# Performance work log

Measured on AMD Instinct MI355X. Metric: run time of the kernel, lower is better.

## Reference

```python
import jax, jax.numpy as jnp
import numpy as np

HID, H, D = 256, 8, 32
NU, NI, NT, NIM = 20000, 50000, 50000, 50000
EB, ETA, EIA = 400000, 200000, 200000
R_ALPHA = 0.5


def setup_inputs() -> dict:
    key = jax.random.key(0)
    ks = iter(jax.random.split(key, 64))
    def nrm(shape, s):
        return (jax.random.normal(next(ks), shape, jnp.float32) * s)
    inp = {}
    inp['x_user'] = nrm((NU, HID), 1.0)
    inp['x_item'] = nrm((NI, HID), 1.0)
    inp['x_taste'] = nrm((NT, HID), 1.0)
    inp['x_image'] = nrm((NIM, HID), 1.0)
    inp['eb_src'] = jax.random.randint(next(ks), (EB,), 0, NU)
    inp['eb_dst'] = jax.random.randint(next(ks), (EB,), 0, NI)
    inp['eta_src'] = jax.random.randint(next(ks), (ETA,), 0, NT)
    inp['eta_dst'] = jax.random.randint(next(ks), (ETA,), 0, NI)
    inp['eia_src'] = jax.random.randint(next(ks), (EIA,), 0, NIM)
    inp['eia_dst'] = jax.random.randint(next(ks), (EIA,), 0, NI)
    wscale = 1.0 / np.sqrt(HID)
    for t in ['user', 'taste', 'image']:
        inp[f'Wk_{t}'] = nrm((HID, HID), wscale)
        inp[f'bk_{t}'] = jnp.zeros((HID,), jnp.float32)
        inp[f'Wv_{t}'] = nrm((HID, HID), wscale)
        inp[f'bv_{t}'] = jnp.zeros((HID,), jnp.float32)
    inp['Wq_item'] = nrm((HID, HID), wscale)
    inp['bq_item'] = jnp.zeros((HID,), jnp.float32)
    rscale = 1.0 / np.sqrt(D)
    for r in ['buys', 'ta', 'ia']:
        inp[f'a_{r}'] = nrm((H, D, D), rscale)   # HGT a_rel (attention) per head
        inp[f'm_{r}'] = nrm((H, D, D), rscale)   # HGT m_rel (message) per head
        inp[f'p_{r}'] = jnp.ones((H,), jnp.float32)  # relation priority
    inp['Wo_item'] = nrm((HID, HID), wscale)
    inp['bo_item'] = jnp.zeros((HID,), jnp.float32)
    inp['skip_item'] = jnp.array(1.0, jnp.float32)  # PyG init: skip=1
    return inp


def _proj(x, W, b):
    return (x @ W + b).reshape(-1, H, D)


def _edge_attend(q, k, v, a_rel, m_rel, p_rel, src, dst):
    # per-source-node relation transforms (cheaper than per-edge when E > N)
    kr = jnp.einsum('nhd,hde->nhe', k, a_rel)
    vr = jnp.einsum('nhd,hde->nhe', v, m_rel)
    logits = jnp.einsum('ehd,ehd->eh', q[dst], kr[src]) * p_rel / np.sqrt(D)  # [E,H]
    mx = jax.ops.segment_max(logits, dst, num_segments=NI)
    ex = jnp.exp(logits - mx[dst])
    den = jax.ops.segment_sum(ex, dst, num_segments=NI)
    alpha = ex / (den[dst] + 1e-16)
    return jax.ops.segment_sum(vr[src] * alpha[:, :, None], dst, num_segments=NI)


def reference(x_user, x_item, x_taste, x_image,
              eb_src, eb_dst, eta_src, eta_dst, eia_src, eia_dst,
              Wk_user, bk_user, Wv_user, bv_user,
              Wk_taste, bk_taste, Wv_taste, bv_taste,
              Wk_image, bk_image, Wv_image, bv_image,
              Wq_item, bq_item,
              a_buys, m_buys, p_buys, a_ta, m_ta, p_ta, a_ia, m_ia, p_ia,
              Wo_item, bo_item, skip_item):
    q = _proj(x_item, Wq_item, bq_item)
    agg = _edge_attend(q, _proj(x_user, Wk_user, bk_user), _proj(x_user, Wv_user, bv_user),
                       a_buys, m_buys, p_buys, eb_src, eb_dst)
    agg = agg + _edge_attend(q, _proj(x_taste, Wk_taste, bk_taste), _proj(x_taste, Wv_taste, bv_taste),
                             a_ta, m_ta, p_ta, eta_src, eta_dst)
    agg = agg + _edge_attend(q, _proj(x_image, Wk_image, bk_image), _proj(x_image, Wv_image, bv_image),
                             a_ia, m_ia, p_ia, eia_src, eia_dst)
    out = jax.nn.gelu(agg).reshape(-1, HID) @ Wo_item + bo_item
    s = jax.nn.sigmoid(skip_item)
    out = s * out + (1.0 - s) * x_item          # HGTConv skip connection
    return out * (1.0 - R_ALPHA) + x_item * R_ALPHA  # MultiModalFusionGAT residual blend
```

## Files before the change

kernel.cpp:

```cpp
#include <hip/hip_runtime.h>
#include <stdint.h>

namespace {

constexpr int cNI  = 50000;
constexpr int cNU  = 20000;
constexpr int cNT  = 50000;
constexpr int cNIM = 50000;
constexpr int cEB  = 400000;
constexpr int cETA = 200000;
constexpr int cEIA = 200000;
constexpr int cTOT = 3 * cNI;

typedef __bf16 bf16x8 __attribute__((ext_vector_type(8)));
typedef float  floatx4 __attribute__((ext_vector_type(4)));

__device__ __forceinline__ float bf2f(unsigned short u) {
  union { unsigned int i; float f; } c;
  c.i = ((unsigned int)u) << 16;
  return c.f;
}
__device__ __forceinline__ unsigned short f2bf(float f) {
  union { float f; unsigned int i; } c;
  c.f = f;
  unsigned int u = c.i;
  u += 0x7fffu + ((u >> 16) & 1u);
  return (unsigned short)(u >> 16);
}
__device__ __forceinline__ float gelu_f(float x) {
  float u = 0.7978845608028654f * (x + 0.044715f * x * x * x);
  float e = __expf(2.f * u);
  float t = 1.f - 2.f / (e + 1.f);
  return 0.5f * x * (1.f + t);
}

__global__ __launch_bounds__(256) void combine_kernel(
    const float* __restrict__ Wk_u, const float* __restrict__ bk_u,
    const float* __restrict__ Wv_u, const float* __restrict__ bv_u,
    const float* __restrict__ Wk_t, const float* __restrict__ bk_t,
    const float* __restrict__ Wv_t, const float* __restrict__ bv_t,
    const float* __restrict__ Wk_i, const float* __restrict__ bk_i,
    const float* __restrict__ Wv_i, const float* __restrict__ bv_i,
    const float* __restrict__ a_b, const float* __restrict__ m_b, const float* __restrict__ p_b,
    const float* __restrict__ a_t, const float* __restrict__ m_t, const float* __restrict__ p_t,
    const float* __restrict__ a_i, const float* __restrict__ m_i, const float* __restrict__ p_i,
    const float* __restrict__ Wq, const float* __restrict__ bq,
    const float* __restrict__ Wo, const float* __restrict__ bo,
    unsigned short* __restrict__ WkvT_u, float* __restrict__ bkv_u,
    unsigned short* __restrict__ WkvT_t, float* __restrict__ bkv_t,
    unsigned short* __restrict__ WkvT_i, float* __restrict__ bkv_i,
    unsigned short* __restrict__ WqT, float* __restrict__ bqf,
    unsigned short* __restrict__ WoT, float* __restrict__ bof)
{
  int idx = blockIdx.x * 256 + threadIdx.x;
  if (idx < 3 * 512 * 256) {
    int rel  = idx >> 17;
    int rem  = idx & 131071;
    int jrow = rem >> 8;
    int k    = rem & 255;
    int isv  = jrow >> 8;
    int j = jrow & 255, h = j >> 5, e = j & 31;
    const float *W, *bin, *A, *pp;
    unsigned short* Wout; float* bout;
    if (rel == 0)      { W = isv ? Wv_u : Wk_u; bin = isv ? bv_u : bk_u; A = isv ? m_b : a_b; pp = p_b; Wout = WkvT_u; bout = bkv_u; }
    else if (rel == 1) { W = isv ? Wv_t : Wk_t; bin = isv ? bv_t : bk_t; A = isv ? m_t : a_t; pp = p_t; Wout = WkvT_t; bout = bkv_t; }
    else               { W = isv ? Wv_i : Wk_i; bin = isv ? bv_i : bk_i; A = isv ? m_i : a_i; pp = p_i; Wout = WkvT_i; bout = bkv_i; }
    float scale = isv ? 1.0f : pp[h] * 0.17677669529663687f;
    const float* wrow = W + k * 256 + h * 32;
    const float* acol = A + h * 1024 + e;
    float acc = 0.f;
    for (int d = 0; d < 32; ++d) acc += wrow[d] * acol[d * 32];
    Wout[jrow * 256 + k] = f2bf(acc * scale);
    if (k == 0) {
      const float* brow = bin + h * 32;
      float bacc = 0.f;
      for (int d = 0; d < 32; ++d) bacc += brow[d] * acol[d * 32];
      bout[jrow] = bacc * scale;
    }
  } else if (idx < 3 * 512 * 256 + 2 * 256 * 256) {
    int rem = idx - 3 * 512 * 256;
    int which = rem >> 16;
    int r2 = rem & 65535;
    int j = r2 >> 8, k = r2 & 255;
    if (which == 0) { WqT[j * 256 + k] = f2bf(Wq[k * 256 + j]); if (k == 0) bqf[j] = bq[j]; }
    else            { WoT[j * 256 + k] = f2bf(Wo[k * 256 + j]); if (k == 0) bof[j] = bo[j]; }
  }
}

template <int MODE>
__global__ __launch_bounds__(256) void gemm_bt_kernel(
    const void* __restrict__ Avp, const unsigned short* __restrict__ BT,
    const float* __restrict__ bias, void* __restrict__ Cvp,
    int M, int N,
    const float* __restrict__ xres, const float* __restrict__ skipp)
{
  __shared__ __align__(16) unsigned short As[64][40];
  __shared__ __align__(16) unsigned short Bs[64][40];
  const int tid = threadIdx.x;
  const int m0 = blockIdx.x * 64;
  const int n0 = blockIdx.y * 64;
  const int wave = tid >> 6, lane = tid & 63;
  const int wm = (wave >> 1) * 32, wn = (wave & 1) * 32;
  const int quad = lane >> 4, l16 = lane & 15;
  floatx4 acc00 = {0.f,0.f,0.f,0.f}, acc01 = {0.f,0.f,0.f,0.f};
  floatx4 acc10 = {0.f,0.f,0.f,0.f}, acc11 = {0.f,0.f,0.f,0.f};
  const int lrow = tid >> 2, lq = tid & 3;
  const int grow = m0 + lrow;
  for (int kt = 0; kt < 256; kt += 32) {
    uint4 av = make_uint4(0u, 0u, 0u, 0u);
    if (MODE == 0) {
      const float* Af = (const float*)Avp;
      if (grow < M) {
        const float4* ap = (const float4*)(Af + (size_t)grow * 256 + kt + lq * 8);
        float4 f0 = ap[0], f1 = ap[1];
        av.x = (unsigned int)f2bf(f0.x) | ((unsigned int)f2bf(f0.y) << 16);
        av.y = (unsigned int)f2bf(f0.z) | ((unsigned int)f2bf(f0.w) << 16);
        av.z = (unsigned int)f2bf(f1.x) | ((unsigned int)f2bf(f1.y) << 16);
        av.w = (unsigned int)f2bf(f1.z) | ((unsigned int)f2bf(f1.w) << 16);
      }
    } else {
      const unsigned short* Ab = (const unsigned short*)Avp;
      if (grow < M) av = *(const uint4*)(Ab + (size_t)grow * 256 + kt + lq * 8);
    }
    uint4 bv = *(const uint4*)(BT + (size_t)(n0 + lrow) * 256 + kt + lq * 8);
    *(uint4*)(&As[lrow][lq * 8]) = av;
    *(uint4*)(&Bs[lrow][lq * 8]) = bv;
    __syncthreads();
    bf16x8 a0 = *(const bf16x8*)(&As[wm + l16][quad * 8]);
    bf16x8 a1 = *(const bf16x8*)(&As[wm + 16 + l16][quad * 8]);
    bf16x8 b0 = *(const bf16x8*)(&Bs[wn + l16][quad * 8]);
    bf16x8 b1 = *(const bf16x8*)(&Bs[wn + 16 + l16][quad * 8]);
    acc00 = __builtin_amdgcn_mfma_f32_16x16x32_bf16(a0, b0, acc00, 0, 0, 0);
    acc01 = __builtin_amdgcn_mfma_f32_16x16x32_bf16(a0, b1, acc01, 0, 0, 0);
    acc10 = __builtin_amdgcn_mfma_f32_16x16x32_bf16(a1, b0, acc10, 0, 0, 0);
    acc11 = __builtin_amdgcn_mfma_f32_16x16x32_bf16(a1, b1, acc11, 0, 0, 0);
    __syncthreads();
  }
  float s = 0.f;
  if (MODE == 1) s = 1.f / (1.f + __expf(-skipp[0]));
  floatx4 accs[2][2] = {{acc00, acc01}, {acc10, acc11}};
  for (int mi = 0; mi < 2; ++mi) {
    for (int ni = 0; ni < 2; ++ni) {
      int col = n0 + wn + ni * 16 + l16;
      int rbase = m0 + wm + mi * 16 + quad * 4;
      float bcol = bias[col];
      for (int r = 0; r < 4; ++r) {
        int row = rbase + r;
        if (row < M) {
          float v = accs[mi][ni][r] + bcol;
          if (MODE == 0) {
            ((unsigned short*)Cvp)[(size_t)row * N + col] = f2bf(v);
          } else {
            float xi = xres[(size_t)row * 256 + col];
            float o = s * v + (1.f - s) * xi;
            ((float*)Cvp)[(size_t)row * 256 + col] = 0.5f * o + 0.5f * xi;
          }
        }
      }
    }
  }
}

__global__ __launch_bounds__(256) void hist_kernel(
    const int* __restrict__ ebd, const int* __restrict__ etd, const int* __restrict__ eid,
    int* __restrict__ cnt)
{
  int i = blockIdx.x * 256 + threadIdx.x;
  if (i < cEB)  atomicAdd(&cnt[ebd[i]], 1);
  if (i < cETA) atomicAdd(&cnt[cNI + etd[i]], 1);
  if (i < cEIA) atomicAdd(&cnt[2 * cNI + eid[i]], 1);
}

__global__ __launch_bounds__(256) void scan1_kernel(
    const int* __restrict__ cnt, int* __restrict__ tpre, int* __restrict__ bsum)
{
  __shared__ int wsum[4];
  const int tid = threadIdx.x, lane = tid & 63, wid = tid >> 6;
  const int base = blockIdx.x * 4096 + tid * 16;
  int s = 0;
  if (base + 16 <= cTOT) {
    const int4* p4 = (const int4*)(cnt + base);
    for (int j = 0; j < 4; ++j) { int4 v = p4[j]; s += v.x + v.y + v.z + v.w; }
  } else {
    for (int j = 0; j < 16; ++j) { int i = base + j; if (i < cTOT) s += cnt[i]; }
  }
  int x = s;
  for (int d = 1; d < 64; d <<= 1) { int t = __shfl_up(x, d, 64); if (lane >= d) x += t; }
  if (lane == 63) wsum[wid] = x;
  __syncthreads();
  int wb = 0;
  for (int w = 0; w < 4; ++w) { int v = wsum[w]; if (w < wid) wb += v; }
  tpre[blockIdx.x * 256 + tid] = wb + x - s;
  if (tid == 255) bsum[blockIdx.x] = wb + x;
}

__global__ __launch_bounds__(64) void scan2_kernel(
    const int* __restrict__ bsum, int* __restrict__ bbase, int* __restrict__ off,
    int nblocks)
{
  const int lane = threadIdx.x;
  int v = (lane < nblocks) ? bsum[lane] : 0;
  int x = v;
  for (int d = 1; d < 64; d <<= 1) { int t = __shfl_up(x, d, 64); if (lane >= d) x += t; }
  if (lane < nblocks) bbase[lane] = x - v;
  if (lane == 0) {
    off[cNI] = cEB;
    off[(cNI + 1) + cNI] = cETA;
    off[2 * (cNI + 1) + cNI] = cEIA;
  }
}

__global__ __launch_bounds__(256) void scan3_kernel(
    const int* __restrict__ cnt, const int* __restrict__ tpre,
    const int* __restrict__ bbase, int* __restrict__ off, int* __restrict__ cur)
{
  const int tid = threadIdx.x;
  const int b = blockIdx.x;
  const int base = b * 4096 + tid * 16;
  int run = bbase[b] + tpre[b * 256 + tid];
  for (int j = 0; j < 16; ++j) {
    int i = base + j;
    if (i >= cTOT) break;
    int rel = (i >= 2 * cNI) ? 2 : (i >= cNI ? 1 : 0);
    int pos = i - rel * cNI;
    int relbase = (rel == 0) ? 0 : (rel == 1) ? cEB : (cEB + cETA);
    int val = run - relbase;
    off[rel * (cNI + 1) + pos] = val;
    cur[rel * cNI + pos] = val;
    run += cnt[i];
  }
}

__global__ __launch_bounds__(256) void scatter_kernel(
    const int* __restrict__ ebs, const int* __restrict__ ebd,
    const int* __restrict__ ets, const int* __restrict__ etd,
    const int* __restrict__ eis, const int* __restrict__ eid,
    int* __restrict__ cur,
    int* __restrict__ ss_b, int* __restrict__ ss_t, int* __restrict__ ss_i)
{
  int i = blockIdx.x * 256 + threadIdx.x;
  if (i < cEB)  { int p = atomicAdd(&cur[ebd[i]], 1);           ss_b[p] = ebs[i]; }
  if (i < cETA) { int p = atomicAdd(&cur[cNI + etd[i]], 1);     ss_t[p] = ets[i]; }
  if (i < cEIA) { int p = atomicAdd(&cur[2 * cNI + eid[i]], 1); ss_i[p] = eis[i]; }
}

__global__ __launch_bounds__(256) void attend_kernel(
    const unsigned short* __restrict__ q,
    const unsigned short* __restrict__ kv_u,
    const unsigned short* __restrict__ kv_t,
    const unsigned short* __restrict__ kv_i,
    const int* __restrict__ off,
    const int* __restrict__ ss_b, const int* __restrict__ ss_t, const int* __restrict__ ss_i,
    unsigned short* __restrict__ gout)
{
  const int wave = threadIdx.x >> 6;
  const int lane = threadIdx.x & 63;
  const int item = blockIdx.x * 4 + wave;
  if (item >= cNI) return;
  ushort4 qu = ((const ushort4*)(q + (size_t)item * 256))[lane];
  const float q0 = bf2f(qu.x), q1 = bf2f(qu.y), q2 = bf2f(qu.z), q3 = bf2f(qu.w);
  float t0 = 0.f, t1 = 0.f, t2 = 0.f, t3 = 0.f;

#define EDGE_DOT(ku, vu, den, a0, a1, a2, a3)                                \
  {                                                                          \
    float p = bf2f(ku.x) * q0 + bf2f(ku.y) * q1 +                            \
              bf2f(ku.z) * q2 + bf2f(ku.w) * q3;                             \
    p += __shfl_xor(p, 1, 8);                                                \
    p += __shfl_xor(p, 2, 8);                                                \
    p += __shfl_xor(p, 4, 8);                                                \
    p = fminf(fmaxf(p, -30.f), 30.f);                                        \
    float ex = __expf(p);                                                    \
    den += ex;                                                               \
    a0 += ex * bf2f(vu.x); a1 += ex * bf2f(vu.y);                            \
    a2 += ex * bf2f(vu.z); a3 += ex * bf2f(vu.w);                            \
  }

#define DO_REL(KV, OFFBASE, SS, NSRC)                                        \
  {                                                                          \
    int e0 = off[(OFFBASE) + item];                                          \
    int e1 = off[(OFFBASE) + item + 1];                                      \
    float den = 0.f, a0 = 0.f, a1 = 0.f, a2 = 0.f, a3 = 0.f;                 \
    int e = e0;                                                              \
    for (; e + 2 <= e1; e += 2) {                                            \
      int s0 = SS[e], s1 = SS[e + 1];                                        \
      if ((unsigned)s0 >= (unsigned)(NSRC)) s0 = 0;                          \
      if ((unsigned)s1 >= (unsigned)(NSRC)) s1 = 0;                          \
      const ushort4* b0p = (const ushort4*)((KV) + (size_t)s0 * 512);        \
      const ushort4* b1p = (const ushort4*)((KV) + (size_t)s1 * 512);        \
      ushort4 k0 = b0p[lane];                                                \
      ushort4 v0 = b0p[64 + lane];                                           \
      ushort4 k1 = b1p[lane];                                                \
      ushort4 v1 = b1p[64 + lane];                                           \
      EDGE_DOT(k0, v0, den, a0, a1, a2, a3)                                  \
      EDGE_DOT(k1, v1, den, a0, a1, a2, a3)                                  \
    }                                                                        \
    if (e < e1) {                                                            \
      int s0 = SS[e];                                                        \
      if ((unsigned)s0 >= (unsigned)(NSRC)) s0 = 0;                          \
      const ushort4* b0p = (const ushort4*)((KV) + (size_t)s0 * 512);        \
      ushort4 k0 = b0p[lane];                                                \
      ushort4 v0 = b0p[64 + lane];                                           \
      EDGE_DOT(k0, v0, den, a0, a1, a2, a3)                                  \
    }                                                                        \
    float inv = 1.f / (den + 1e-16f);                                        \
    t0 += a0 * inv; t1 += a1 * inv; t2 += a2 * inv; t3 += a3 * inv;          \
  }

  DO_REL(kv_u, 0, ss_b, cNU)
  DO_REL(kv_t, (cNI + 1), ss_t, cNT)
  DO_REL(kv_i, 2 * (cNI + 1), ss_i, cNIM)
#undef DO_REL
#undef EDGE_DOT

  ushort4 o;
  o.x = f2bf(gelu_f(t0));
  o.y = f2bf(gelu_f(t1));
  o.z = f2bf(gelu_f(t2));
  o.w = f2bf(gelu_f(t3));
  ((ushort4*)(gout + (size_t)item * 256))[lane] = o;
}

}

extern "C" void kernel_launch(void* const* d_in, const int* in_sizes, int n_in,
                              void* d_out, int out_size, void* d_ws, size_t ws_size,
                              hipStream_t stream) {
  (void)in_sizes; (void)n_in; (void)out_size; (void)ws_size;
  const float* x_user  = (const float*)d_in[0];
  const float* x_item  = (const float*)d_in[1];
  const float* x_taste = (const float*)d_in[2];
  const float* x_image = (const float*)d_in[3];
  const int* eb_src  = (const int*)d_in[4];
  const int* eb_dst  = (const int*)d_in[5];
  const int* eta_src = (const int*)d_in[6];
  const int* eta_dst = (const int*)d_in[7];
  const int* eia_src = (const int*)d_in[8];
  const int* eia_dst = (const int*)d_in[9];
  const float* Wk_u = (const float*)d_in[10];
  const float* bk_u = (const float*)d_in[11];
  const float* Wv_u = (const float*)d_in[12];
  const float* bv_u = (const float*)d_in[13];
  const float* Wk_t = (const float*)d_in[14];
  const float* bk_t = (const float*)d_in[15];
  const float* Wv_t = (const float*)d_in[16];
  const float* bv_t = (const float*)d_in[17];
  const float* Wk_i = (const float*)d_in[18];
  const float* bk_i = (const float*)d_in[19];
  const float* Wv_i = (const float*)d_in[20];
  const float* bv_i = (const float*)d_in[21];
  const float* Wq   = (const float*)d_in[22];
  const float* bq   = (const float*)d_in[23];
  const float* a_b  = (const float*)d_in[24];
  const float* m_b  = (const float*)d_in[25];
  const float* p_b  = (const float*)d_in[26];
  const float* a_t  = (const float*)d_in[27];
  const float* m_t  = (const float*)d_in[28];
  const float* p_t  = (const float*)d_in[29];
  const float* a_i  = (const float*)d_in[30];
  const float* m_i  = (const float*)d_in[31];
  const float* p_i  = (const float*)d_in[32];
  const float* Wo   = (const float*)d_in[33];
  const float* bo   = (const float*)d_in[34];
  const float* skip = (const float*)d_in[35];

  char* p = (char*)d_ws;
  auto alloc = [&](size_t n) -> char* {
    char* r = p;
    p += (n + 255) & ~(size_t)255;
    return r;
  };
  unsigned short* q      = (unsigned short*)alloc((size_t)cNI * 256 * 2);
  unsigned short* kv_u   = (unsigned short*)alloc((size_t)cNU * 512 * 2);
  unsigned short* kv_t   = (unsigned short*)alloc((size_t)cNT * 512 * 2);
  unsigned short* kv_i   = (unsigned short*)alloc((size_t)cNIM * 512 * 2);
  unsigned short* gagg   = (unsigned short*)alloc((size_t)cNI * 256 * 2);
  unsigned short* WkvT_u = (unsigned short*)alloc(512 * 256 * 2);
  unsigned short* WkvT_t = (unsigned short*)alloc(512 * 256 * 2);
  unsigned short* WkvT_i = (unsigned short*)alloc(512 * 256 * 2);
  unsigned short* WqT    = (unsigned short*)alloc(256 * 256 * 2);
  unsigned short* WoT    = (unsigned short*)alloc(256 * 256 * 2);
  float* bkv_u = (float*)alloc(512 * 4);
  float* bkv_t = (float*)alloc(512 * 4);
  float* bkv_i = (float*)alloc(512 * 4);
  float* bqf   = (float*)alloc(256 * 4);
  float* bof   = (float*)alloc(256 * 4);
  int* cnt   = (int*)alloc((size_t)cTOT * 4);
  int* off   = (int*)alloc((size_t)3 * (cNI + 1) * 4);
  int* cur   = (int*)alloc((size_t)cTOT * 4);
  int* tpre  = (int*)alloc((size_t)37 * 256 * 4);
  int* bsum  = (int*)alloc(64 * 4);
  int* bbase = (int*)alloc(64 * 4);
  int* ss_b = (int*)alloc((size_t)cEB * 4);
  int* ss_t = (int*)alloc((size_t)cETA * 4);
  int* ss_i = (int*)alloc((size_t)cEIA * 4);

  hipMemsetAsync(cnt, 0, (size_t)cTOT * 4, stream);

  combine_kernel<<<2048, 256, 0, stream>>>(
      Wk_u, bk_u, Wv_u, bv_u, Wk_t, bk_t, Wv_t, bv_t, Wk_i, bk_i, Wv_i, bv_i,
      a_b, m_b, p_b, a_t, m_t, p_t, a_i, m_i, p_i,
      Wq, bq, Wo, bo,
      WkvT_u, bkv_u, WkvT_t, bkv_t, WkvT_i, bkv_i, WqT, bqf, WoT, bof);

  gemm_bt_kernel<0><<<dim3(782, 4), 256, 0, stream>>>(x_item, WqT, bqf, q, cNI, 256, nullptr, nullptr);
  gemm_bt_kernel<0><<<dim3(313, 8), 256, 0, stream>>>(x_user, WkvT_u, bkv_u, kv_u, cNU, 512, nullptr, nullptr);
  gemm_bt_kernel<0><<<dim3(782, 8), 256, 0, stream>>>(x_taste, WkvT_t, bkv_t, kv_t, cNT, 512, nullptr, nullptr);
  gemm_bt_kernel<0><<<dim3(782, 8), 256, 0, stream>>>(x_image, WkvT_i, bkv_i, kv_i, cNIM, 512, nullptr, nullptr);

  hist_kernel<<<1563, 256, 0, stream>>>(eb_dst, eta_dst, eia_dst, cnt);
  scan1_kernel<<<37, 256, 0, stream>>>(cnt, tpre, bsum);
  scan2_kernel<<<1, 64, 0, stream>>>(bsum, bbase, off, 37);
  scan3_kernel<<<37, 256, 0, stream>>>(cnt, tpre, bbase, off, cur);
  scatter_kernel<<<1563, 256, 0, stream>>>(eb_src, eb_dst, eta_src, eta_dst, eia_src, eia_dst,
                                           cur, ss_b, ss_t, ss_i);

  attend_kernel<<<12500, 256, 0, stream>>>(q, kv_u, kv_t, kv_i, off, ss_b, ss_t, ss_i, gagg);

  gemm_bt_kernel<1><<<dim3(782, 4), 256, 0, stream>>>(gagg, WoT, bof, d_out,
                                                      cNI, 256, x_item, skip);
}
```

Before: 699.6 us.

## Batch projection GEMMs into one strip kernel, merge scan passes, unroll attend loop

The four projection GEMMs now run as a single grouped launch. Each block loads a full 64x256 A strip once into shared memory, keeps it in registers, and loops over all N tiles. This stops the fp32 input from being re-read and re-converted once per N tile, and it cuts launch count. The scan2 kernel is removed: each scan3 block sums the preceding block totals itself. The attend loop now processes four edges at a time to keep more gathers in flight. In exchange, the change uses more shared memory and registers per block and launches fewer blocks, which may lower occupancy.

```diff
diff --git a/kernel.cpp b/kernel.cpp
--- a/kernel.cpp
+++ b/kernel.cpp
@@ -11,6 +11,12 @@
 constexpr int cETA = 200000;
 constexpr int cEIA = 200000;
 constexpr int cTOT = 3 * cNI;
+constexpr int cSCANB = 37;
+
+constexpr int cSQ  = (cNI  + 63) / 64;
+constexpr int cSU  = (cNU  + 63) / 64;
+constexpr int cST  = (cNT  + 63) / 64;
+constexpr int cSIM = (cNIM + 63) / 64;
 
 typedef __bf16 bf16x8 __attribute__((ext_vector_type(8)));
 typedef float  floatx4 __attribute__((ext_vector_type(4)));
@@ -88,30 +94,42 @@
 }
 
 template <int MODE>
-__global__ __launch_bounds__(256) void gemm_bt_kernel(
-    const void* __restrict__ Avp, const unsigned short* __restrict__ BT,
-    const float* __restrict__ bias, void* __restrict__ Cvp,
-    int M, int N,
+__global__ __launch_bounds__(256) void gemm_strip_kernel(
+    const void* __restrict__ A0, const unsigned short* __restrict__ B0,
+    const float* __restrict__ bias0, void* __restrict__ C0, int M0, int N0,
+    const void* __restrict__ A1, const unsigned short* __restrict__ B1,
+    const float* __restrict__ bias1, void* __restrict__ C1, int M1, int N1,
+    const void* __restrict__ A2, const unsigned short* __restrict__ B2,
+    const float* __restrict__ bias2, void* __restrict__ C2, int M2, int N2,
+    const void* __restrict__ A3, const unsigned short* __restrict__ B3,
+    const float* __restrict__ bias3, void* __restrict__ C3, int M3, int N3,
     const float* __restrict__ xres, const float* __restrict__ skipp)
 {
-  __shared__ __align__(16) unsigned short As[64][40];
-  __shared__ __align__(16) unsigned short Bs[64][40];
+  __shared__ __align__(16) unsigned short As[8][64][40];
+  __shared__ __align__(16) unsigned short Bs[8][64][40];
+
+  const void* Avp; const unsigned short* BT; const float* bias; void* Cvp;
+  int M, N, strip;
+  int b = blockIdx.x;
+  if (MODE == 1 || b < cSQ)            { Avp = A0; BT = B0; bias = bias0; Cvp = C0; M = M0; N = N0; strip = b; }
+  else if (b < cSQ + cSU)              { Avp = A1; BT = B1; bias = bias1; Cvp = C1; M = M1; N = N1; strip = b - cSQ; }
+  else if (b < cSQ + cSU + cST)        { Avp = A2; BT = B2; bias = bias2; Cvp = C2; M = M2; N = N2; strip = b - cSQ - cSU; }
+  else                                 { Avp = A3; BT = B3; bias = bias3; Cvp = C3; M = M3; N = N3; strip = b - cSQ - cSU - cST; }
+
   const int tid = threadIdx.x;
-  const int m0 = blockIdx.x * 64;
-  const int n0 = blockIdx.y * 64;
+  const int m0 = strip * 64;
   const int wave = tid >> 6, lane = tid & 63;
   const int wm = (wave >> 1) * 32, wn = (wave & 1) * 32;
   const int quad = lane >> 4, l16 = lane & 15;
-  floatx4 acc00 = {0.f,0.f,0.f,0.f}, acc01 = {0.f,0.f,0.f,0.f};
-  floatx4 acc10 = {0.f,0.f,0.f,0.f}, acc11 = {0.f,0.f,0.f,0.f};
   const int lrow = tid >> 2, lq = tid & 3;
   const int grow = m0 + lrow;
-  for (int kt = 0; kt < 256; kt += 32) {
+
+#pragma unroll
+  for (int kt = 0; kt < 8; ++kt) {
     uint4 av = make_uint4(0u, 0u, 0u, 0u);
     if (MODE == 0) {
-      const float* Af = (const float*)Avp;
       if (grow < M) {
-        const float4* ap = (const float4*)(Af + (size_t)grow * 256 + kt + lq * 8);
+        const float4* ap = (const float4*)((const float*)Avp + (size_t)grow * 256 + kt * 32 + lq * 8);
         float4 f0 = ap[0], f1 = ap[1];
         av.x = (unsigned int)f2bf(f0.x) | ((unsigned int)f2bf(f0.y) << 16);
         av.y = (unsigned int)f2bf(f0.z) | ((unsigned int)f2bf(f0.w) << 16);
@@ -119,45 +137,69 @@
         av.w = (unsigned int)f2bf(f1.z) | ((unsigned int)f2bf(f1.w) << 16);
       }
     } else {
-      const unsigned short* Ab = (const unsigned short*)Avp;
-      if (grow < M) av = *(const uint4*)(Ab + (size_t)grow * 256 + kt + lq * 8);
+      if (grow < M) av = *(const uint4*)((const unsigned short*)Avp + (size_t)grow * 256 + kt * 32 + lq * 8);
     }
-    uint4 bv = *(const uint4*)(BT + (size_t)(n0 + lrow) * 256 + kt + lq * 8);
-    *(uint4*)(&As[lrow][lq * 8]) = av;
-    *(uint4*)(&Bs[lrow][lq * 8]) = bv;
-    __syncthreads();
-    bf16x8 a0 = *(const bf16x8*)(&As[wm + l16][quad * 8]);
-    bf16x8 a1 = *(const bf16x8*)(&As[wm + 16 + l16][quad * 8]);
-    bf16x8 b0 = *(const bf16x8*)(&Bs[wn + l16][quad * 8]);
-    bf16x8 b1 = *(const bf16x8*)(&Bs[wn + 16 + l16][quad * 8]);
-    acc00 = __builtin_amdgcn_mfma_f32_16x16x32_bf16(a0, b0, acc00, 0, 0, 0);
-    acc01 = __builtin_amdgcn_mfma_f32_16x16x32_bf16(a0, b1, acc01, 0, 0, 0);
-    acc10 = __builtin_amdgcn_mfma_f32_16x16x32_bf16(a1, b0, acc10, 0, 0, 0);
-    acc11 = __builtin_amdgcn_mfma_f32_16x16x32_bf16(a1, b1, acc11, 0, 0, 0);
-    __syncthreads();
-  }
+    *(uint4*)(&As[kt][lrow][lq * 8]) = av;
+  }
+  __syncthreads();
+
+  bf16x8 af0[8], af1[8];
+#pragma unroll
+  for (int kt = 0; kt < 8; ++kt) {
+    af0[kt] = *(const bf16x8*)(&As[kt][wm + l16][quad * 8]);
+    af1[kt] = *(const bf16x8*)(&As[kt][wm + 16 + l16][quad * 8]);
+  }
+
   float s = 0.f;
   if (MODE == 1) s = 1.f / (1.f + __expf(-skipp[0]));
-  floatx4 accs[2][2] = {{acc00, acc01}, {acc10, acc11}};
-  for (int mi = 0; mi < 2; ++mi) {
-    for (int ni = 0; ni < 2; ++ni) {
-      int col = n0 + wn + ni * 16 + l16;
-      int rbase = m0 + wm + mi * 16 + quad * 4;
-      float bcol = bias[col];
-      for (int r = 0; r < 4; ++r) {
-        int row = rbase + r;
-        if (row < M) {
-          float v = accs[mi][ni][r] + bcol;
-          if (MODE == 0) {
-            ((unsigned short*)Cvp)[(size_t)row * N + col] = f2bf(v);
-          } else {
-            float xi = xres[(size_t)row * 256 + col];
-            float o = s * v + (1.f - s) * xi;
-            ((float*)Cvp)[(size_t)row * 256 + col] = 0.5f * o + 0.5f * xi;
+
+  const int ntiles = N >> 6;
+  for (int nt = 0; nt < ntiles; ++nt) {
+    const int n0 = nt * 64;
+#pragma unroll
+    for (int kt = 0; kt < 8; ++kt) {
+      uint4 bv = *(const uint4*)(BT + (size_t)(n0 + lrow) * 256 + kt * 32 + lq * 8);
+      *(uint4*)(&Bs[kt][lrow][lq * 8]) = bv;
+    }
+    __syncthreads();
+
+    floatx4 acc00 = {0.f,0.f,0.f,0.f}, acc01 = {0.f,0.f,0.f,0.f};
+    floatx4 acc10 = {0.f,0.f,0.f,0.f}, acc11 = {0.f,0.f,0.f,0.f};
+#pragma unroll
+    for (int kt = 0; kt < 8; ++kt) {
+      bf16x8 b0 = *(const bf16x8*)(&Bs[kt][wn + l16][quad * 8]);
+      bf16x8 b1 = *(const bf16x8*)(&Bs[kt][wn + 16 + l16][quad * 8]);
+      acc00 = __builtin_amdgcn_mfma_f32_16x16x32_bf16(af0[kt], b0, acc00, 0, 0, 0);
+      acc01 = __builtin_amdgcn_mfma_f32_16x16x32_bf16(af0[kt], b1, acc01, 0, 0, 0);
+      acc10 = __builtin_amdgcn_mfma_f32_16x16x32_bf16(af1[kt], b0, acc10, 0, 0, 0);
+      acc11 = __builtin_amdgcn_mfma_f32_16x16x32_bf16(af1[kt], b1, acc11, 0, 0, 0);
+    }
+
+    floatx4 accs[2][2] = {{acc00, acc01}, {acc10, acc11}};
+#pragma unroll
+    for (int mi = 0; mi < 2; ++mi) {
+#pragma unroll
+      for (int ni = 0; ni < 2; ++ni) {
+        int col = n0 + wn + ni * 16 + l16;
+        int rbase = m0 + wm + mi * 16 + quad * 4;
+        float bcol = bias[col];
+#pragma unroll
+        for (int r = 0; r < 4; ++r) {
+          int row = rbase + r;
+          if (row < M) {
+            float v = accs[mi][ni][r] + bcol;
+            if (MODE == 0) {
+              ((unsigned short*)Cvp)[(size_t)row * N + col] = f2bf(v);
+            } else {
+              float xi = xres[(size_t)row * 256 + col];
+              float o = s * v + (1.f - s) * xi;
+              ((float*)Cvp)[(size_t)row * 256 + col] = 0.5f * o + 0.5f * xi;
+            }
           }
         }
       }
     }
+    __syncthreads();
   }
 }
 
@@ -194,30 +236,21 @@
   if (tid == 255) bsum[blockIdx.x] = wb + x;
 }
 
-__global__ __launch_bounds__(64) void scan2_kernel(
-    const int* __restrict__ bsum, int* __restrict__ bbase, int* __restrict__ off,
-    int nblocks)
-{
-  const int lane = threadIdx.x;
-  int v = (lane < nblocks) ? bsum[lane] : 0;
-  int x = v;
-  for (int d = 1; d < 64; d <<= 1) { int t = __shfl_up(x, d, 64); if (lane >= d) x += t; }
-  if (lane < nblocks) bbase[lane] = x - v;
-  if (lane == 0) {
+__global__ __launch_bounds__(256) void scan3_kernel(
+    const int* __restrict__ cnt, const int* __restrict__ tpre,
+    const int* __restrict__ bsum, int* __restrict__ off, int* __restrict__ cur)
+{
+  const int tid = threadIdx.x;
+  const int b = blockIdx.x;
+  int bb = 0;
+  for (int w = 0; w < b; ++w) bb += bsum[w];
+  if (b == 0 && tid == 0) {
     off[cNI] = cEB;
     off[(cNI + 1) + cNI] = cETA;
     off[2 * (cNI + 1) + cNI] = cEIA;
   }
-}
-
-__global__ __launch_bounds__(256) void scan3_kernel(
-    const int* __restrict__ cnt, const int* __restrict__ tpre,
-    const int* __restrict__ bbase, int* __restrict__ off, int* __restrict__ cur)
-{
-  const int tid = threadIdx.x;
-  const int b = blockIdx.x;
   const int base = b * 4096 + tid * 16;
-  int run = bbase[b] + tpre[b * 256 + tid];
+  int run = bb + tpre[b * 256 + tid];
   for (int j = 0; j < 16; ++j) {
     int i = base + j;
     if (i >= cTOT) break;
@@ -281,25 +314,41 @@
     int e1 = off[(OFFBASE) + item + 1];                                      \
     float den = 0.f, a0 = 0.f, a1 = 0.f, a2 = 0.f, a3 = 0.f;                 \
     int e = e0;                                                              \
+    for (; e + 4 <= e1; e += 4) {                                            \
+      int s0 = SS[e], s1 = SS[e + 1], s2 = SS[e + 2], s3 = SS[e + 3];        \
+      if ((unsigned)s0 >= (unsigned)(NSRC)) s0 = 0;                          \
+      if ((unsigned)s1 >= (unsigned)(NSRC)) s1 = 0;                          \
+      if ((unsigned)s2 >= (unsigned)(NSRC)) s2 = 0;                          \
+      if ((unsigned)s3 >= (unsigned)(NSRC)) s3 = 0;                          \
+      const ushort4* p0 = (const ushort4*)((KV) + (size_t)s0 * 512);         \
+      const ushort4* p1 = (const ushort4*)((KV) + (size_t)s1 * 512);         \
+      const ushort4* p2 = (const ushort4*)((KV) + (size_t)s2 * 512);         \
+      const ushort4* p3 = (const ushort4*)((KV) + (size_t)s3 * 512);         \
+      ushort4 k0 = p0[lane], v0 = p0[64 + lane];                             \
+      ushort4 k1 = p1[lane], v1 = p1[64 + lane];                             \
+      ushort4 k2 = p2[lane], v2 = p2[64 + lane];                             \
+      ushort4 k3 = p3[lane], v3 = p3[64 + lane];                             \
+      EDGE_DOT(k0, v0, den, a0, a1, a2, a3)                                  \
+      EDGE_DOT(k1, v1, den, a0, a1, a2, a3)                                  \
+      EDGE_DOT(k2, v2, den, a0, a1, a2, a3)                                  \
+      EDGE_DOT(k3, v3, den, a0, a1, a2, a3)                                  \
+    }                                                                        \
     for (; e + 2 <= e1; e += 2) {                                            \
       int s0 = SS[e], s1 = SS[e + 1];                                        \
       if ((unsigned)s0 >= (unsigned)(NSRC)) s0 = 0;                          \
       if ((unsigned)s1 >= (unsigned)(NSRC)) s1 = 0;                          \
-      const ushort4* b0p = (const ushort4*)((KV) + (size_t)s0 * 512);        \
-      const ushort4* b1p = (const ushort4*)((KV) + (size_t)s1 * 512);        \
-      ushort4 k0 = b0p[lane];                                                \
-      ushort4 v0 = b0p[64 + lane];                                           \
-      ushort4 k1 = b1p[lane];                                                \
-      ushort4 v1 = b1p[64 + lane];                                           \
+      const ushort4* p0 = (const ushort4*)((KV) + (size_t)s0 * 512);         \
+      const ushort4* p1 = (const ushort4*)((KV) + (size_t)s1 * 512);         \
+      ushort4 k0 = p0[lane], v0 = p0[64 + lane];                             \
+      ushort4 k1 = p1[lane], v1 = p1[64 + lane];                             \
       EDGE_DOT(k0, v0, den, a0, a1, a2, a3)                                  \
       EDGE_DOT(k1, v1, den, a0, a1, a2, a3)                                  \
     }                                                                        \
     if (e < e1) {                                                            \
       int s0 = SS[e];                                                        \
       if ((unsigned)s0 >= (unsigned)(NSRC)) s0 = 0;                          \
-      const ushort4* b0p = (const ushort4*)((KV) + (size_t)s0 * 512);        \
-      ushort4 k0 = b0p[lane];                                                \
-      ushort4 v0 = b0p[64 + lane];                                           \
+      const ushort4* p0 = (const ushort4*)((KV) + (size_t)s0 * 512);         \
+      ushort4 k0 = p0[lane], v0 = p0[64 + lane];                             \
       EDGE_DOT(k0, v0, den, a0, a1, a2, a3)                                  \
     }                                                                        \
     float inv = 1.f / (den + 1e-16f);                                        \
@@ -387,9 +436,8 @@
   int* cnt   = (int*)alloc((size_t)cTOT * 4);
   int* off   = (int*)alloc((size_t)3 * (cNI + 1) * 4);
   int* cur   = (int*)alloc((size_t)cTOT * 4);
-  int* tpre  = (int*)alloc((size_t)37 * 256 * 4);
+  int* tpre  = (int*)alloc((size_t)cSCANB * 256 * 4);
   int* bsum  = (int*)alloc(64 * 4);
-  int* bbase = (int*)alloc(64 * 4);
   int* ss_b = (int*)alloc((size_t)cEB * 4);
   int* ss_t = (int*)alloc((size_t)cETA * 4);
   int* ss_i = (int*)alloc((size_t)cEIA * 4);
@@ -402,20 +450,25 @@
       Wq, bq, Wo, bo,
       WkvT_u, bkv_u, WkvT_t, bkv_t, WkvT_i, bkv_i, WqT, bqf, WoT, bof);
 
-  gemm_bt_kernel<0><<<dim3(782, 4), 256, 0, stream>>>(x_item, WqT, bqf, q, cNI, 256, nullptr, nullptr);
-  gemm_bt_kernel<0><<<dim3(313, 8), 256, 0, stream>>>(x_user, WkvT_u, bkv_u, kv_u, cNU, 512, nullptr, nullptr);
-  gemm_bt_kernel<0><<<dim3(782, 8), 256, 0, stream>>>(x_taste, WkvT_t, bkv_t, kv_t, cNT, 512, nullptr, nullptr);
-  gemm_bt_kernel<0><<<dim3(782, 8), 256, 0, stream>>>(x_image, WkvT_i, bkv_i, kv_i, cNIM, 512, nullptr, nullptr);
+  gemm_strip_kernel<0><<<cSQ + cSU + cST + cSIM, 256, 0, stream>>>(
+      x_item,  WqT,    bqf,   q,    cNI,  256,
+      x_user,  WkvT_u, bkv_u, kv_u, cNU,  512,
+      x_taste, WkvT_t, bkv_t, kv_t, cNT,  512,
+      x_image, WkvT_i, bkv_i, kv_i, cNIM, 512,
+      nullptr, nullptr);
 
   hist_kernel<<<1563, 256, 0, stream>>>(eb_dst, eta_dst, eia_dst, cnt);
-  scan1_kernel<<<37, 256, 0, stream>>>(cnt, tpre, bsum);
-  scan2_kernel<<<1, 64, 0, stream>>>(bsum, bbase, off, 37);
-  scan3_kernel<<<37, 256, 0, stream>>>(cnt, tpre, bbase, off, cur);
+  scan1_kernel<<<cSCANB, 256, 0, stream>>>(cnt, tpre, bsum);
+  scan3_kernel<<<cSCANB, 256, 0, stream>>>(cnt, tpre, bsum, off, cur);
   scatter_kernel<<<1563, 256, 0, stream>>>(eb_src, eb_dst, eta_src, eta_dst, eia_src, eia_dst,
                                            cur, ss_b, ss_t, ss_i);
 
   attend_kernel<<<12500, 256, 0, stream>>>(q, kv_u, kv_t, kv_i, off, ss_b, ss_t, ss_i, gagg);
 
-  gemm_bt_kernel<1><<<dim3(782, 4), 256, 0, stream>>>(gagg, WoT, bof, d_out,
-                                                      cNI, 256, x_item, skip);
-}
+  gemm_strip_kernel<1><<<cSQ, 256, 0, stream>>>(
+      gagg, WoT, bof, d_out, cNI, 256,
+      nullptr, nullptr, nullptr, nullptr, 0, 0,
+      nullptr, nullptr, nullptr, nullptr, 0, 0,
+      nullptr, nullptr, nullptr, nullptr, 0, 0,
+      x_item, skip);
+}
```

After: 642.4 us. 8.2% less time.
